# Performance work log

Hardware: AMD Instinct MI355X
Metric: run time of the kernel (lower is better)

Reference implementation:

```python
import jax, jax.numpy as jnp
import numpy as np

B, C, H, W = 4, 256, 64, 64
CI = 3
TEMPERATURE = 0.0001 * 5
EPS = 2.220446049250313e-16  # sys.float_info.epsilon


def _nearest_up4(x):
    # nn.Upsample(scale_factor=4, mode='nearest'): [B,C,H,W] -> [B,C,4H,4W]
    return jnp.repeat(jnp.repeat(x, 4, axis=2), 4, axis=3)


def _avg_pool2(x):
    # AvgPool2d(kernel=2, stride=2, pad=0)
    b, c, h, w = x.shape
    return x.reshape(b, c, h // 2, 2, w // 2, 2).mean(axis=(3, 5))


def _center_norm(feats):
    # subtract per-channel spatial mean, then L2-normalize over channels per position
    b, c, h, w = feats.shape
    t = feats.reshape(b, c, h * w)
    t = t - t.mean(axis=-1, keepdims=True)
    n = jnp.linalg.norm(t, axis=1, keepdims=True) + EPS
    return t / n  # [B,C,HW]


def setup_inputs() -> dict:
    key = jax.random.key(0)
    k1, k2, k3 = jax.random.split(key, 3)
    return {
        "x_feats": jax.random.normal(k1, (B, C, H, W), jnp.float32),
        "y_feats": jax.random.normal(k2, (B, C, H, W), jnp.float32),
        "y_img": jax.random.uniform(k3, (B, CI, 4 * H, 4 * W), jnp.float32),
    }


def reference(x_feats, y_feats, y_img):
    b, c, h, w = x_feats.shape
    hw = h * w
    theta = _center_norm(x_feats)  # [B,C,HW]
    phi = _center_norm(y_feats)    # [B,C,HW]
    f = jnp.einsum('bcm,bcn->bmn', theta, phi)  # dense correlation [B,HW,HW]
    loss_feat_pair = jnp.mean(jnp.abs(theta - phi))  # F.l1_loss(theta, phi)
    # WTA_scale_weight == 1 -> WTA branch bypassed, just temperature scaling
    f_wta = f / TEMPERATURE
    f_div_c = jax.nn.softmax(f_wta, axis=-1)  # [B,HW,HW]
    # warped features: f_div_C @ y_feats^T
    b_lab = y_feats.reshape(b, c, hw)
    y = jnp.einsum('bmn,bcn->bcm', f_div_c, b_lab).reshape(b, c, h, w)
    # soft-argmax coordinates
    xc = (jnp.arange(hw) % w).astype(x_feats.dtype)   # [HW]
    yc = (jnp.arange(hw) // w).astype(x_feats.dtype)  # [HW]
    coords_x = f_div_c @ xc  # [B,HW]
    coords_y = f_div_c @ yc  # [B,HW]
    coords1 = jnp.stack([coords_x, coords_y], axis=1).reshape(b, 2, h, w)
    coords0 = jnp.stack([xc, yc], axis=0).reshape(1, 2, h, w)
    flow = _nearest_up4(coords1 - coords0)  # [B,2,4H,4W]
    # image warping branch (y_img is not None)
    yi = _avg_pool2(_avg_pool2(y_img))  # [B,CI,H,W]
    ci = yi.shape[1]
    yi_flat = yi.reshape(b, ci, hw)
    y_img_attn = jnp.einsum('bmn,bcn->bmc', f_div_c, yi_flat)  # [B,HW,CI]
    f_div_c_v = jax.nn.softmax(jnp.swapaxes(f_wta, 1, 2), axis=-1)
    y_img_cyc = jnp.einsum('bmn,bnc->bcm', f_div_c_v, y_img_attn).reshape(b, ci, h, w)
    y_img_out = jnp.swapaxes(y_img_attn, 1, 2).reshape(b, ci, h, w)
    return (y, flow, _nearest_up4(y_img_out), _nearest_up4(y_img_cyc), loss_feat_pair)
```

## Files before the change

kernel.cpp:

```cpp
#include <hip/hip_runtime.h>
#include <math.h>

#define HW   4096
#define NCH  256
#define NB   4

constexpr float TEMP  = (float)(0.0001 * 5.0);
constexpr float INV_T = 1.0f / TEMP;
constexpr float EPSN  = 2.220446049250313e-16f;

typedef __attribute__((ext_vector_type(8))) _Float16 f16x8;
typedef __attribute__((ext_vector_type(4))) float    f32x4;

constexpr size_t OFF_YT    = 0;
constexpr size_t OFF_YI    = OFF_YT    + (size_t)NB*HW*NCH;
constexpr size_t OFF_MEAN  = OFF_YI    + (size_t)NB*3*HW;
constexpr size_t OFF_RNORM = OFF_MEAN  + (size_t)2*NB*NCH;
constexpr size_t OFF_NSQP  = OFF_RNORM + (size_t)2*NB*HW;
constexpr size_t OFF_F     = OFF_NSQP  + (size_t)2*NB*8*HW;
constexpr size_t OFF_YP    = OFF_F     + (size_t)HW*HW;
constexpr size_t OFF_ROWP  = OFF_YP;
constexpr size_t OFF_COLP  = OFF_YP + (size_t)32*7*HW;
constexpr size_t OFF_RMAX  = OFF_YP    + (size_t)8*NCH*HW;
constexpr size_t OFF_RSUM  = OFF_RMAX  + HW;
constexpr size_t OFF_CMAX  = OFF_RSUM  + HW;
constexpr size_t OFF_CSUM  = OFF_CMAX  + HW;
constexpr size_t OFF_COORD = OFF_CSUM  + HW;
constexpr size_t OFF_ATTN  = OFF_COORD + (size_t)NB*2*HW;
constexpr size_t OFF_CYC   = OFF_ATTN  + (size_t)NB*HW*3;
constexpr size_t OFF_CYCP  = OFF_CYC   + (size_t)NB*3*HW;
constexpr size_t OFF_LOSSP = OFF_CYCP  + (size_t)32*3*HW;
constexpr size_t OFF_F16   = OFF_LOSSP + 1024;

constexpr size_t OUT_Y    = 0;
constexpr size_t OUT_FLOW = (size_t)NB*NCH*HW;
constexpr size_t OUT_IMG  = OUT_FLOW + (size_t)NB*2*256*256;
constexpr size_t OUT_CYCO = OUT_IMG  + (size_t)NB*3*256*256;
constexpr size_t OUT_LOSS = OUT_CYCO + (size_t)NB*3*256*256;

__device__ __forceinline__ void gload16(const void* g, void* l) {
    __builtin_amdgcn_global_load_lds(
        (const __attribute__((address_space(1))) unsigned int*)g,
        (__attribute__((address_space(3))) unsigned int*)l, 16, 0, 0);
}

__global__ void mean_kernel(const float* __restrict__ xf, const float* __restrict__ yf,
                            float* __restrict__ means) {
    const float* src = (blockIdx.y == 0 ? xf : yf) + (size_t)blockIdx.x * HW;
    float s = 0.f;
    for (int i = threadIdx.x; i < HW; i += 256) s += src[i];
    __shared__ float red[256];
    red[threadIdx.x] = s; __syncthreads();
    for (int st = 128; st > 0; st >>= 1) {
        if (threadIdx.x < st) red[threadIdx.x] += red[threadIdx.x + st];
        __syncthreads();
    }
    if (threadIdx.x == 0) means[blockIdx.y * (NB*NCH) + blockIdx.x] = red[0] * (1.0f / HW);
}

__global__ void nsq_partial_kernel(const float* __restrict__ xf, const float* __restrict__ yf,
                                   const float* __restrict__ means, float* __restrict__ part) {
    int t = blockIdx.z >> 2, b = blockIdx.z & 3;
    int m = blockIdx.x * 256 + threadIdx.x;
    int c0 = blockIdx.y * 32;
    const float* src = (t == 0 ? xf : yf) + (size_t)b * NCH * HW;
    const float* mn = means + t * (NB*NCH) + b * NCH;
    float acc = 0.f;
    for (int c = c0; c < c0 + 32; ++c) {
        float v = src[(size_t)c * HW + m] - mn[c];
        acc += v * v;
    }
    part[(((size_t)t*NB + b) * 8 + blockIdx.y) * HW + m] = acc;
}

__global__ void nsq_combine_kernel(const float* __restrict__ part, float* __restrict__ rnorms) {
    int t = blockIdx.y >> 2, b = blockIdx.y & 3;
    int m = blockIdx.x * 256 + threadIdx.x;
    const float* p = part + ((size_t)t*NB + b) * 8 * HW + m;
    float s = 0.f;
    for (int k = 0; k < 8; ++k) s += p[(size_t)k * HW];
    rnorms[((size_t)t*NB + b) * HW + m] = 1.0f / (sqrtf(s) + EPSN);
}

__global__ void ycast_kernel(const float* __restrict__ yf, _Float16* __restrict__ yf16) {
    size_t i = ((size_t)blockIdx.x * 256 + threadIdx.x) * 8;
    const float4* s = (const float4*)(yf + i);
    float4 v0 = s[0], v1 = s[1];
    f16x8 o;
    o[0]=(_Float16)v0.x; o[1]=(_Float16)v0.y; o[2]=(_Float16)v0.z; o[3]=(_Float16)v0.w;
    o[4]=(_Float16)v1.x; o[5]=(_Float16)v1.y; o[6]=(_Float16)v1.z; o[7]=(_Float16)v1.w;
    *(f16x8*)(yf16 + i) = o;
}

__global__ void prep_kernel(const float* __restrict__ xf, const float* __restrict__ yf,
                            const float* __restrict__ means,
                            _Float16* __restrict__ th, _Float16* __restrict__ tl,
                            _Float16* __restrict__ ph, _Float16* __restrict__ pl, int b) {
    __shared__ float tile[32][33];
    int t = blockIdx.z;
    int c0 = blockIdx.x * 32, m0 = blockIdx.y * 32;
    const float* src = (t == 0 ? xf : yf) + (size_t)b * NCH * HW;
    const float* mn  = means + t * (NB*NCH) + b * NCH;
    int tx = threadIdx.x & 31, ty = threadIdx.x >> 5;
    for (int i = ty; i < 32; i += 8)
        tile[i][tx] = src[(size_t)(c0 + i) * HW + m0 + tx] - mn[c0 + i];
    __syncthreads();
    _Float16* H = (t == 0 ? th : ph);
    _Float16* L = (t == 0 ? tl : pl);
    for (int i = ty; i < 32; i += 8) {
        float v = tile[tx][i];
        _Float16 h = (_Float16)v;
        _Float16 l = (_Float16)(v - (float)h);
        H[(size_t)(m0 + i)*NCH + c0 + tx] = h;
        L[(size_t)(m0 + i)*NCH + c0 + tx] = l;
    }
}

__global__ void avgpool_kernel(const float* __restrict__ yimg, float* __restrict__ yi) {
    size_t idx = (size_t)blockIdx.x * 256 + threadIdx.x;
    int m  = (int)(idx & (HW - 1));
    int bc = (int)(idx >> 12);
    int h = m >> 6, w = m & 63;
    const float* p = yimg + (size_t)bc * 65536 + (size_t)(h*4) * 256 + w*4;
    float s = 0.f;
    #pragma unroll
    for (int dy = 0; dy < 4; ++dy) {
        #pragma unroll
        for (int dx = 0; dx < 4; ++dx) s += p[dy*256 + dx];
    }
    yi[idx] = s * (1.0f/16.0f);
}

__global__ __launch_bounds__(256) void gemm_f_kernel(
        const _Float16* __restrict__ th, const _Float16* __restrict__ tl,
        const _Float16* __restrict__ ph, const _Float16* __restrict__ pl,
        const float* __restrict__ rnorms, const float* __restrict__ yi,
        float* __restrict__ f, float* __restrict__ rowp, float* __restrict__ colp,
        int b) {
    __shared__ char lds[4][8192];
    int tid  = threadIdx.x;
    int lane = tid & 63;
    int w = tid >> 6, wm = w >> 1, wn = w & 1;
    int m0 = blockIdx.y * 128, n0 = blockIdx.x * 128;

    int o0 = tid * 16, o1 = o0 + 4096;
    int r0 = o0 >> 6, s0 = (o0 >> 4) & 3, g0 = s0 ^ ((r0 >> 1) & 3);
    int r1 = o1 >> 6, s1 = (o1 >> 4) & 3, g1 = s1 ^ ((r1 >> 1) & 3);
    size_t ga0 = (size_t)(n0 + r0)*NCH + g0*8;
    size_t ga1 = (size_t)(n0 + r1)*NCH + g1*8;
    size_t gb0 = (size_t)(m0 + r0)*NCH + g0*8;
    size_t gb1 = (size_t)(m0 + r1)*NCH + g1*8;

    int fra = wm*64 + (lane & 15);
    int frb = wn*64 + (lane & 15);
    int ks  = lane >> 4;

    f32x4 acc[4][4];
    #pragma unroll
    for (int i = 0; i < 4; ++i)
        #pragma unroll
        for (int j = 0; j < 4; ++j) acc[i][j] = (f32x4){0.f, 0.f, 0.f, 0.f};

    for (int kt = 0; kt < 8; ++kt) {
        int k0 = kt * 32;
        gload16(ph + ga0 + k0, &lds[0][o0]);
        gload16(ph + ga1 + k0, &lds[0][o1]);
        gload16(pl + ga0 + k0, &lds[1][o0]);
        gload16(pl + ga1 + k0, &lds[1][o1]);
        gload16(th + gb0 + k0, &lds[2][o0]);
        gload16(th + gb1 + k0, &lds[2][o1]);
        gload16(tl + gb0 + k0, &lds[3][o0]);
        gload16(tl + gb1 + k0, &lds[3][o1]);
        __syncthreads();

        f16x8 ah[4], al[4], bh[4], bl[4];
        #pragma unroll
        for (int i = 0; i < 4; ++i) {
            int rowa = fra + i*16;
            int offa = rowa*64 + ((ks ^ ((rowa >> 1) & 3)) << 4);
            ah[i] = *(const f16x8*)&lds[0][offa];
            al[i] = *(const f16x8*)&lds[1][offa];
            int rowb = frb + i*16;
            int offb = rowb*64 + ((ks ^ ((rowb >> 1) & 3)) << 4);
            bh[i] = *(const f16x8*)&lds[2][offb];
            bl[i] = *(const f16x8*)&lds[3][offb];
        }
        #pragma unroll
        for (int i = 0; i < 4; ++i)
            #pragma unroll
            for (int j = 0; j < 4; ++j) {
                acc[i][j] = __builtin_amdgcn_mfma_f32_16x16x32_f16(ah[i], bh[j], acc[i][j], 0, 0, 0);
                acc[i][j] = __builtin_amdgcn_mfma_f32_16x16x32_f16(ah[i], bl[j], acc[i][j], 0, 0, 0);
                acc[i][j] = __builtin_amdgcn_mfma_f32_16x16x32_f16(al[i], bh[j], acc[i][j], 0, 0, 0);
            }
        __syncthreads();
    }

    const float* rnx = rnorms + (size_t)b * HW;
    const float* rny = rnorms + (size_t)(NB + b) * HW;
    int mg[4];  float rxv[4];
    #pragma unroll
    for (int j = 0; j < 4; ++j) {
        mg[j] = m0 + wn*64 + j*16 + (lane & 15);
        rxv[j] = rnx[mg[j]];
    }
    int nl0 = wm*64 + (lane >> 4)*4;
    #pragma unroll
    for (int i = 0; i < 4; ++i)
        #pragma unroll
        for (int r = 0; r < 4; ++r) {
            float ry = rny[n0 + nl0 + i*16 + r];
            #pragma unroll
            for (int j = 0; j < 4; ++j) acc[i][j][r] *= rxv[j] * ry;
        }

    #pragma unroll
    for (int j = 0; j < 4; ++j)
        #pragma unroll
        for (int i = 0; i < 4; ++i)
            *(f32x4*)&f[(size_t)mg[j]*HW + n0 + nl0 + i*16] = acc[i][j];

    float* S     = (float*)&lds[0][0];
    float* rowm  = S;
    float* sums6 = S + 256;
    float* colm  = S + 1792;
    float* colsm = S + 2048;

    #pragma unroll
    for (int j = 0; j < 4; ++j) {
        float v = acc[0][j][0];
        #pragma unroll
        for (int i = 0; i < 4; ++i)
            #pragma unroll
            for (int r = 0; r < 4; ++r) v = fmaxf(v, acc[i][j][r]);
        v = fmaxf(v, __shfl_xor(v, 16));
        v = fmaxf(v, __shfl_xor(v, 32));
        if ((lane >> 4) == 0) rowm[wm*128 + wn*64 + j*16 + lane] = v;
    }
    #pragma unroll
    for (int i = 0; i < 4; ++i)
        #pragma unroll
        for (int r = 0; r < 4; ++r) {
            float v = fmaxf(fmaxf(acc[i][0][r], acc[i][1][r]),
                            fmaxf(acc[i][2][r], acc[i][3][r]));
            #pragma unroll
            for (int d = 1; d < 16; d <<= 1) v = fmaxf(v, __shfl_xor(v, d));
            if ((lane & 15) == 0) colm[wn*128 + wm*64 + i*16 + (lane >> 4)*4 + r] = v;
        }
    __syncthreads();

    float bm[4];
    #pragma unroll
    for (int j = 0; j < 4; ++j) {
        int ml = wn*64 + j*16 + (lane & 15);
        bm[j] = fmaxf(rowm[ml], rowm[128 + ml]);
    }
    float a6[4][6];
    #pragma unroll
    for (int j = 0; j < 4; ++j)
        #pragma unroll
        for (int q = 0; q < 6; ++q) a6[j][q] = 0.f;
    const float* yib = yi + (size_t)b * 3 * HW;
    #pragma unroll
    for (int i = 0; i < 4; ++i)
        #pragma unroll
        for (int r = 0; r < 4; ++r) {
            int ng = n0 + nl0 + i*16 + r;
            float xc = (float)(ng & 63), yc = (float)(ng >> 6);
            float y0 = yib[ng], y1 = yib[HW + ng], y2 = yib[2*HW + ng];
            #pragma unroll
            for (int j = 0; j < 4; ++j) {
                float e = __expf((acc[i][j][r] - bm[j]) * INV_T);
                a6[j][0] += e;      a6[j][1] += e*xc; a6[j][2] += e*yc;
                a6[j][3] += e*y0;   a6[j][4] += e*y1; a6[j][5] += e*y2;
            }
        }
    #pragma unroll
    for (int j = 0; j < 4; ++j)
        #pragma unroll
        for (int q = 0; q < 6; ++q) {
            float v = a6[j][q];
            v += __shfl_xor(v, 16);
            v += __shfl_xor(v, 32);
            if ((lane >> 4) == 0) sums6[(wm*128 + wn*64 + j*16 + lane)*6 + q] = v;
        }
    #pragma unroll
    for (int i = 0; i < 4; ++i)
        #pragma unroll
        for (int r = 0; r < 4; ++r) {
            int nl = wm*64 + i*16 + (lane >> 4)*4 + r;
            float cm = fmaxf(colm[nl], colm[128 + nl]);
            float cs = 0.f;
            #pragma unroll
            for (int j = 0; j < 4; ++j) cs += __expf((acc[i][j][r] - cm) * INV_T);
            #pragma unroll
            for (int d = 1; d < 16; d <<= 1) cs += __shfl_xor(cs, d);
            if ((lane & 15) == 0) colsm[wn*128 + nl] = cs;
        }
    __syncthreads();

    if (tid < 128) {
        int ml = tid;
        float m2 = fmaxf(rowm[ml], rowm[128 + ml]);
        rowp[((size_t)blockIdx.x*7 + 0)*HW + m0 + ml] = m2;
        #pragma unroll
        for (int q = 0; q < 6; ++q)
            rowp[((size_t)blockIdx.x*7 + 1 + q)*HW + m0 + ml] =
                sums6[ml*6 + q] + sums6[(128 + ml)*6 + q];
    } else {
        int nl = tid - 128;
        float c2 = fmaxf(colm[nl], colm[128 + nl]);
        colp[((size_t)blockIdx.y*2 + 0)*HW + n0 + nl] = c2;
        colp[((size_t)blockIdx.y*2 + 1)*HW + n0 + nl] = colsm[nl] + colsm[128 + nl];
    }
}

__global__ void row_combine_kernel(const float* __restrict__ rowp,
        float* __restrict__ rmax, float* __restrict__ rsuminv,
        float* __restrict__ coords, float* __restrict__ attn, int b) {
    int m = blockIdx.x * 256 + threadIdx.x;
    float gm = -3.0e38f;
    for (int t = 0; t < 32; ++t) gm = fmaxf(gm, rowp[((size_t)t*7)*HW + m]);
    float S=0, CX=0, CY=0, A0=0, A1=0, A2=0;
    for (int t = 0; t < 32; ++t) {
        const float* p = rowp + (size_t)t*7*HW + m;
        float wgt = __expf((p[0] - gm) * INV_T);
        S  += p[1*HW] * wgt; CX += p[2*HW] * wgt; CY += p[3*HW] * wgt;
        A0 += p[4*HW] * wgt; A1 += p[5*HW] * wgt; A2 += p[6*HW] * wgt;
    }
    float inv = 1.0f / S;
    rmax[m] = gm; rsuminv[m] = inv;
    coords[((size_t)b*2 + 0)*HW + m] = CX * inv;
    coords[((size_t)b*2 + 1)*HW + m] = CY * inv;
    attn[((size_t)b*HW + m)*3 + 0] = A0 * inv;
    attn[((size_t)b*HW + m)*3 + 1] = A1 * inv;
    attn[((size_t)b*HW + m)*3 + 2] = A2 * inv;
}

__global__ void col_combine_kernel(const float* __restrict__ colp,
        float* __restrict__ cmax, float* __restrict__ csuminv) {
    int n = blockIdx.x * 256 + threadIdx.x;
    float gm = -3.0e38f;
    for (int t = 0; t < 32; ++t) gm = fmaxf(gm, colp[((size_t)t*2)*HW + n]);
    float S = 0.f;
    for (int t = 0; t < 32; ++t) {
        const float* p = colp + (size_t)t*2*HW + n;
        S += p[1*HW] * __expf((p[0] - gm) * INV_T);
    }
    cmax[n] = gm;
    csuminv[n] = 1.0f / S;
}

__global__ __launch_bounds__(512) void gemm_y_kernel(const float* __restrict__ f,
        const float* __restrict__ rmax, const _Float16* __restrict__ yf16,
        float* __restrict__ yp, int b) {
    __shared__ __align__(16) char ldsA[8192];
    __shared__ __align__(16) char ldsB[16384];
    int tid  = threadIdx.x;
    int lane = tid & 63;
    int w = tid >> 6, wm = w >> 2, wn = w & 3;
    int m0 = blockIdx.x * 128;
    int ks = blockIdx.y;
    const _Float16* Yb = yf16 + (size_t)b * NCH * HW;

    int ar = tid >> 2, akc = tid & 3;
    int aoff = ar*64 + ((akc ^ ((ar >> 1) & 3)) << 4);
    float arm = rmax[m0 + ar];
    const float* frow = f + (size_t)(m0 + ar)*HW + akc*8;

    int o0 = tid*16, o1 = o0 + 8192;
    int br0 = o0 >> 6, bs0 = (o0 >> 4) & 3, bg0 = bs0 ^ ((br0 >> 1) & 3);
    int br1 = o1 >> 6, bs1 = (o1 >> 4) & 3, bg1 = bs1 ^ ((br1 >> 1) & 3);
    size_t gb0 = (size_t)br0*HW + bg0*8;
    size_t gb1 = (size_t)br1*HW + bg1*8;

    int fra = wm*64 + (lane & 15);
    int frb = wn*64 + (lane & 15);
    int kslot = lane >> 4;

    f32x4 acc[4][4];
    #pragma unroll
    for (int i = 0; i < 4; ++i)
        #pragma unroll
        for (int j = 0; j < 4; ++j) acc[i][j] = (f32x4){0.f, 0.f, 0.f, 0.f};

    for (int k0 = ks*512; k0 < ks*512 + 512; k0 += 32) {
        gload16(Yb + gb0 + k0, &ldsB[o0]);
        gload16(Yb + gb1 + k0, &ldsB[o1]);
        const float4* fp = (const float4*)(frow + k0);
        float4 v0 = fp[0], v1 = fp[1];
        f16x8 pk;
        pk[0] = (_Float16)__expf((v0.x - arm) * INV_T);
        pk[1] = (_Float16)__expf((v0.y - arm) * INV_T);
        pk[2] = (_Float16)__expf((v0.z - arm) * INV_T);
        pk[3] = (_Float16)__expf((v0.w - arm) * INV_T);
        pk[4] = (_Float16)__expf((v1.x - arm) * INV_T);
        pk[5] = (_Float16)__expf((v1.y - arm) * INV_T);
        pk[6] = (_Float16)__expf((v1.z - arm) * INV_T);
        pk[7] = (_Float16)__expf((v1.w - arm) * INV_T);
        *(f16x8*)&ldsA[aoff] = pk;
        __syncthreads();

        f16x8 af[4], bf[4];
        #pragma unroll
        for (int i = 0; i < 4; ++i) {
            int rowa = fra + i*16;
            af[i] = *(const f16x8*)&ldsA[rowa*64 + ((kslot ^ ((rowa >> 1) & 3)) << 4)];
            int rowb = frb + i*16;
            bf[i] = *(const f16x8*)&ldsB[rowb*64 + ((kslot ^ ((rowb >> 1) & 3)) << 4)];
        }
        #pragma unroll
        for (int i = 0; i < 4; ++i)
            #pragma unroll
            for (int j = 0; j < 4; ++j)
                acc[i][j] = __builtin_amdgcn_mfma_f32_16x16x32_f16(af[i], bf[j], acc[i][j], 0, 0, 0);
        __syncthreads();
    }

    #pragma unroll
    for (int i = 0; i < 4; ++i) {
        int m = m0 + wm*64 + i*16 + (lane >> 4) * 4;
        #pragma unroll
        for (int j = 0; j < 4; ++j) {
            int c = wn*64 + j*16 + (lane & 15);
            *(f32x4*)(yp + ((size_t)ks*NCH + c)*HW + m) = acc[i][j];
        }
    }
}

__global__ void ycombine_kernel(const float* __restrict__ yp, const float* __restrict__ rsuminv,
                                float* __restrict__ out, int b) {
    size_t idx = (size_t)blockIdx.x * 256 + threadIdx.x;
    int m = (int)(idx & (HW - 1));
    float s = 0.f;
    #pragma unroll
    for (int k = 0; k < 8; ++k) s += yp[(size_t)k*NCH*HW + idx];
    out[OUT_Y + (size_t)b*NCH*HW + idx] = s * rsuminv[m];
}

__global__ __launch_bounds__(256) void cyc_partial_kernel(const float* __restrict__ f,
        const float* __restrict__ cmax, const float* __restrict__ attn,
        float* __restrict__ part, int b) {
    __shared__ float at[128*3];
    int i  = blockIdx.x * 256 + threadIdx.x;
    int j0 = blockIdx.y * 128;
    for (int k = threadIdx.x; k < 384; k += 256)
        at[k] = attn[((size_t)b*HW + j0)*3 + k];
    __syncthreads();
    float cm = cmax[i];
    float a0=0, a1=0, a2=0;
    for (int jj = 0; jj < 128; ++jj) {
        float e = __expf((f[(size_t)(j0+jj)*HW + i] - cm) * INV_T);
        a0 = fmaf(e, at[jj*3+0], a0);
        a1 = fmaf(e, at[jj*3+1], a1);
        a2 = fmaf(e, at[jj*3+2], a2);
    }
    part[((size_t)blockIdx.y*3 + 0)*HW + i] = a0;
    part[((size_t)blockIdx.y*3 + 1)*HW + i] = a1;
    part[((size_t)blockIdx.y*3 + 2)*HW + i] = a2;
}

__global__ void cyc_combine_kernel(const float* __restrict__ part, const float* __restrict__ csuminv,
                                   float* __restrict__ cyc, int b) {
    int i = blockIdx.x * 256 + threadIdx.x;
    int c = blockIdx.y;
    float s = 0.f;
    for (int k = 0; k < 32; ++k) s += part[((size_t)k*3 + c)*HW + i];
    cyc[((size_t)b*3 + c)*HW + i] = s * csuminv[i];
}

__global__ void flow_kernel(const float* __restrict__ coords, float* __restrict__ out) {
    size_t idx = (size_t)blockIdx.x * 256 + threadIdx.x;
    int x4 = (int)(idx & 255);
    int y4 = (int)((idx >> 8) & 255);
    int ch = (int)((idx >> 16) & 1);
    int b  = (int)(idx >> 17);
    int w = x4 >> 2, h = y4 >> 2;
    int m = h*64 + w;
    float c1 = coords[((size_t)b*2 + ch)*HW + m];
    float c0 = (ch == 0) ? (float)w : (float)h;
    out[OUT_FLOW + idx] = c1 - c0;
}

__global__ void imgout_kernel(const float* __restrict__ attn, const float* __restrict__ cyc,
                              float* __restrict__ out) {
    size_t idx = (size_t)blockIdx.x * 256 + threadIdx.x;
    int x4 = (int)(idx & 255);
    int y4 = (int)((idx >> 8) & 255);
    int rest = (int)(idx >> 16);
    int ch = rest % 3, b = rest / 3;
    int m = (y4 >> 2)*64 + (x4 >> 2);
    out[OUT_IMG  + idx] = attn[((size_t)b*HW + m)*3 + ch];
    out[OUT_CYCO + idx] = cyc[((size_t)b*3 + ch)*HW + m];
}

__global__ void loss_partial_kernel(const float* __restrict__ xf, const float* __restrict__ yf,
                                    const float* __restrict__ means, const float* __restrict__ rnorms,
                                    float* __restrict__ part) {
    __shared__ float red[256];
    size_t base = (size_t)blockIdx.x * 4096;
    float s = 0.f;
    for (int k = 0; k < 16; ++k) {
        size_t id = base + (size_t)k*256 + threadIdx.x;
        int m  = (int)(id & (HW - 1));
        int bc = (int)(id >> 12);
        int b  = bc >> 8;
        float th = (xf[id] - means[bc])          * rnorms[(size_t)b*HW + m];
        float ph = (yf[id] - means[NB*NCH + bc]) * rnorms[(size_t)(NB + b)*HW + m];
        s += fabsf(th - ph);
    }
    red[threadIdx.x] = s; __syncthreads();
    for (int st = 128; st > 0; st >>= 1) {
        if (threadIdx.x < st) red[threadIdx.x] += red[threadIdx.x + st];
        __syncthreads();
    }
    if (threadIdx.x == 0) part[blockIdx.x] = red[0];
}

__global__ void loss_final_kernel(const float* __restrict__ part, float* __restrict__ out) {
    __shared__ float red[256];
    float s = 0.f;
    for (int k = threadIdx.x; k < 1024; k += 256) s += part[k];
    red[threadIdx.x] = s; __syncthreads();
    for (int st = 128; st > 0; st >>= 1) {
        if (threadIdx.x < st) red[threadIdx.x] += red[threadIdx.x + st];
        __syncthreads();
    }
    if (threadIdx.x == 0) out[OUT_LOSS] = red[0] * (1.0f / 4194304.0f);
}

extern "C" void kernel_launch(void* const* d_in, const int* in_sizes, int n_in,
                              void* d_out, int out_size, void* d_ws, size_t ws_size,
                              hipStream_t stream) {
    (void)in_sizes; (void)n_in; (void)out_size; (void)ws_size;
    const float* xf   = (const float*)d_in[0];
    const float* yf   = (const float*)d_in[1];
    const float* yimg = (const float*)d_in[2];
    float* out = (float*)d_out;
    float* ws  = (float*)d_ws;

    _Float16* yf16 = (_Float16*)(ws + OFF_YT);
    float* yi      = ws + OFF_YI;
    float* means   = ws + OFF_MEAN;
    float* rnorms  = ws + OFF_RNORM;
    float* nsqp    = ws + OFF_NSQP;
    float* fbuf    = ws + OFF_F;
    float* yp      = ws + OFF_YP;
    float* rowp    = ws + OFF_ROWP;
    float* colp    = ws + OFF_COLP;
    float* rmax    = ws + OFF_RMAX;
    float* rsuminv = ws + OFF_RSUM;
    float* cmax    = ws + OFF_CMAX;
    float* csuminv = ws + OFF_CSUM;
    float* coords  = ws + OFF_COORD;
    float* attn    = ws + OFF_ATTN;
    float* cyc     = ws + OFF_CYC;
    float* cycp    = ws + OFF_CYCP;
    float* lossp   = ws + OFF_LOSSP;
    _Float16* th = (_Float16*)(ws + OFF_F16);
    _Float16* tl = th + (size_t)HW*NCH;
    _Float16* ph = tl + (size_t)HW*NCH;
    _Float16* pl = ph + (size_t)HW*NCH;

    mean_kernel        <<<dim3(NB*NCH, 2),   256, 0, stream>>>(xf, yf, means);
    nsq_partial_kernel <<<dim3(16, 8, 8),    256, 0, stream>>>(xf, yf, means, nsqp);
    nsq_combine_kernel <<<dim3(16, 8),       256, 0, stream>>>(nsqp, rnorms);
    ycast_kernel       <<<2048,              256, 0, stream>>>(yf, yf16);
    avgpool_kernel     <<<NB*3*HW/256,       256, 0, stream>>>(yimg, yi);

    for (int b = 0; b < NB; ++b) {
        prep_kernel        <<<dim3(8, 128, 2), 256, 0, stream>>>(xf, yf, means, th, tl, ph, pl, b);
        gemm_f_kernel      <<<dim3(32, 32),    256, 0, stream>>>(th, tl, ph, pl, rnorms, yi,
                                                                 fbuf, rowp, colp, b);
        row_combine_kernel <<<16,              256, 0, stream>>>(rowp, rmax, rsuminv, coords, attn, b);
        col_combine_kernel <<<16,              256, 0, stream>>>(colp, cmax, csuminv);
        gemm_y_kernel      <<<dim3(32, 8),     512, 0, stream>>>(fbuf, rmax, yf16, yp, b);
        ycombine_kernel    <<<NCH*HW/256,      256, 0, stream>>>(yp, rsuminv, out, b);
        cyc_partial_kernel <<<dim3(16, 32),    256, 0, stream>>>(fbuf, cmax, attn, cycp, b);
        cyc_combine_kernel <<<dim3(16, 3),     256, 0, stream>>>(cycp, csuminv, cyc, b);
    }

    flow_kernel        <<<NB*2*65536/256, 256, 0, stream>>>(coords, out);
    imgout_kernel      <<<NB*3*65536/256, 256, 0, stream>>>(attn, cyc, out);
    loss_partial_kernel<<<1024,           256, 0, stream>>>(xf, yf, means, rnorms, lossp);
    loss_final_kernel  <<<1,              256, 0, stream>>>(lossp, out);
}
```

Measured before the change: 540.0 us.

## Enlarge correlation GEMM tile to 256x256 with 8 waves and staged epilogue

The split-fp16 correlation GEMM now uses 256x256 output tiles with 512 threads (each wave computing 128x64), which halves the number of partial row/column softmax statistics and the combine-kernel loop counts. The epilogue stages the y_img slice into shared memory and merges the column-exp pass into the row-exp loop, so acc is swept one fewer time. The cost is heavier register pressure (32 accumulators per lane) and only 256 blocks per batch, which may leave some of the GPU's compute units underused.

```diff
diff --git a/kernel.cpp b/kernel.cpp
--- a/kernel.cpp
+++ b/kernel.cpp
@@ -131,19 +131,22 @@
     yi[idx] = s * (1.0f/16.0f);
 }
 
-__global__ __launch_bounds__(256) void gemm_f_kernel(
+__global__ __launch_bounds__(512) void gemm_f_kernel(
         const _Float16* __restrict__ th, const _Float16* __restrict__ tl,
         const _Float16* __restrict__ ph, const _Float16* __restrict__ pl,
         const float* __restrict__ rnorms, const float* __restrict__ yi,
         float* __restrict__ f, float* __restrict__ rowp, float* __restrict__ colp,
         int b) {
-    __shared__ char lds[4][8192];
+    __shared__ __align__(16) char lds[4][16384];
     int tid  = threadIdx.x;
     int lane = tid & 63;
-    int w = tid >> 6, wm = w >> 1, wn = w & 1;
-    int m0 = blockIdx.y * 128, n0 = blockIdx.x * 128;
-
-    int o0 = tid * 16, o1 = o0 + 4096;
+    int g    = lane >> 4;
+    int w    = tid >> 6;
+    int wN   = w >> 2;
+    int wM   = w & 3;
+    int n0 = blockIdx.x * 256, m0 = blockIdx.y * 256;
+
+    int o0 = tid * 16, o1 = o0 + 8192;
     int r0 = o0 >> 6, s0 = (o0 >> 4) & 3, g0 = s0 ^ ((r0 >> 1) & 3);
     int r1 = o1 >> 6, s1 = (o1 >> 4) & 3, g1 = s1 ^ ((r1 >> 1) & 3);
     size_t ga0 = (size_t)(n0 + r0)*NCH + g0*8;
@@ -151,13 +154,12 @@
     size_t gb0 = (size_t)(m0 + r0)*NCH + g0*8;
     size_t gb1 = (size_t)(m0 + r1)*NCH + g1*8;
 
-    int fra = wm*64 + (lane & 15);
-    int frb = wn*64 + (lane & 15);
-    int ks  = lane >> 4;
-
-    f32x4 acc[4][4];
-    #pragma unroll
-    for (int i = 0; i < 4; ++i)
+    int fra = wN*128 + (lane & 15);
+    int frb = wM*64  + (lane & 15);
+
+    f32x4 acc[8][4];
+    #pragma unroll
+    for (int i = 0; i < 8; ++i)
         #pragma unroll
         for (int j = 0; j < 4; ++j) acc[i][j] = (f32x4){0.f, 0.f, 0.f, 0.f};
 
@@ -173,43 +175,44 @@
         gload16(tl + gb1 + k0, &lds[3][o1]);
         __syncthreads();
 
-        f16x8 ah[4], al[4], bh[4], bl[4];
-        #pragma unroll
-        for (int i = 0; i < 4; ++i) {
+        f16x8 bh[4], bl[4];
+        #pragma unroll
+        for (int j = 0; j < 4; ++j) {
+            int rowb = frb + j*16;
+            int offb = rowb*64 + ((g ^ ((rowb >> 1) & 3)) << 4);
+            bh[j] = *(const f16x8*)&lds[2][offb];
+            bl[j] = *(const f16x8*)&lds[3][offb];
+        }
+        #pragma unroll
+        for (int i = 0; i < 8; ++i) {
             int rowa = fra + i*16;
-            int offa = rowa*64 + ((ks ^ ((rowa >> 1) & 3)) << 4);
-            ah[i] = *(const f16x8*)&lds[0][offa];
-            al[i] = *(const f16x8*)&lds[1][offa];
-            int rowb = frb + i*16;
-            int offb = rowb*64 + ((ks ^ ((rowb >> 1) & 3)) << 4);
-            bh[i] = *(const f16x8*)&lds[2][offb];
-            bl[i] = *(const f16x8*)&lds[3][offb];
-        }
-        #pragma unroll
-        for (int i = 0; i < 4; ++i)
+            int offa = rowa*64 + ((g ^ ((rowa >> 1) & 3)) << 4);
+            f16x8 ah = *(const f16x8*)&lds[0][offa];
+            f16x8 al = *(const f16x8*)&lds[1][offa];
             #pragma unroll
             for (int j = 0; j < 4; ++j) {
-                acc[i][j] = __builtin_amdgcn_mfma_f32_16x16x32_f16(ah[i], bh[j], acc[i][j], 0, 0, 0);
-                acc[i][j] = __builtin_amdgcn_mfma_f32_16x16x32_f16(ah[i], bl[j], acc[i][j], 0, 0, 0);
-                acc[i][j] = __builtin_amdgcn_mfma_f32_16x16x32_f16(al[i], bh[j], acc[i][j], 0, 0, 0);
+                acc[i][j] = __builtin_amdgcn_mfma_f32_16x16x32_f16(ah, bh[j], acc[i][j], 0, 0, 0);
+                acc[i][j] = __builtin_amdgcn_mfma_f32_16x16x32_f16(ah, bl[j], acc[i][j], 0, 0, 0);
+                acc[i][j] = __builtin_amdgcn_mfma_f32_16x16x32_f16(al, bh[j], acc[i][j], 0, 0, 0);
             }
+        }
         __syncthreads();
     }
 
     const float* rnx = rnorms + (size_t)b * HW;
     const float* rny = rnorms + (size_t)(NB + b) * HW;
-    int mg[4];  float rxv[4];
+    int mg[4]; float rxv[4];
     #pragma unroll
     for (int j = 0; j < 4; ++j) {
-        mg[j] = m0 + wn*64 + j*16 + (lane & 15);
+        mg[j] = m0 + wM*64 + j*16 + (lane & 15);
         rxv[j] = rnx[mg[j]];
     }
-    int nl0 = wm*64 + (lane >> 4)*4;
-    #pragma unroll
-    for (int i = 0; i < 4; ++i)
+    int nlb = wN*128 + g*4;
+    #pragma unroll
+    for (int i = 0; i < 8; ++i)
         #pragma unroll
         for (int r = 0; r < 4; ++r) {
-            float ry = rny[n0 + nl0 + i*16 + r];
+            float ry = rny[n0 + nlb + i*16 + r];
             #pragma unroll
             for (int j = 0; j < 4; ++j) acc[i][j][r] *= rxv[j] * ry;
         }
@@ -217,63 +220,82 @@
     #pragma unroll
     for (int j = 0; j < 4; ++j)
         #pragma unroll
-        for (int i = 0; i < 4; ++i)
-            *(f32x4*)&f[(size_t)mg[j]*HW + n0 + nl0 + i*16] = acc[i][j];
-
-    float* S     = (float*)&lds[0][0];
-    float* rowm  = S;
-    float* sums6 = S + 256;
-    float* colm  = S + 1792;
-    float* colsm = S + 2048;
-
+        for (int i = 0; i < 8; ++i)
+            *(f32x4*)&f[(size_t)mg[j]*HW + n0 + nlb + i*16] = acc[i][j];
+
+    float* yiL = (float*)&lds[0][0];
+    float* rmL = yiL + 768;
+    float* cmL = rmL + 512;
+    float* rsL = cmL + 1024;
+    float* csL = rsL + 3072;
+
+    {
+        const float* yib = yi + (size_t)b * 3 * HW;
+        for (int k = tid; k < 768; k += 512) {
+            int ch = k >> 8, nn = k & 255;
+            yiL[k] = yib[(size_t)ch*HW + n0 + nn];
+        }
+    }
     #pragma unroll
     for (int j = 0; j < 4; ++j) {
         float v = acc[0][j][0];
         #pragma unroll
-        for (int i = 0; i < 4; ++i)
+        for (int i = 0; i < 8; ++i)
             #pragma unroll
             for (int r = 0; r < 4; ++r) v = fmaxf(v, acc[i][j][r]);
         v = fmaxf(v, __shfl_xor(v, 16));
         v = fmaxf(v, __shfl_xor(v, 32));
-        if ((lane >> 4) == 0) rowm[wm*128 + wn*64 + j*16 + lane] = v;
-    }
-    #pragma unroll
-    for (int i = 0; i < 4; ++i)
+        if (lane < 16) rmL[wN*256 + wM*64 + j*16 + lane] = v;
+    }
+    #pragma unroll
+    for (int i = 0; i < 8; ++i)
         #pragma unroll
         for (int r = 0; r < 4; ++r) {
             float v = fmaxf(fmaxf(acc[i][0][r], acc[i][1][r]),
                             fmaxf(acc[i][2][r], acc[i][3][r]));
             #pragma unroll
             for (int d = 1; d < 16; d <<= 1) v = fmaxf(v, __shfl_xor(v, d));
-            if ((lane & 15) == 0) colm[wn*128 + wm*64 + i*16 + (lane >> 4)*4 + r] = v;
+            if ((lane & 15) == 0) cmL[wM*256 + nlb + i*16 + r] = v;
         }
     __syncthreads();
 
+    if (tid < 256) {
+        rmL[tid] = fmaxf(rmL[tid], rmL[256 + tid]);
+    } else {
+        int n = tid - 256;
+        cmL[n] = fmaxf(fmaxf(cmL[n], cmL[256 + n]), fmaxf(cmL[512 + n], cmL[768 + n]));
+    }
+    __syncthreads();
+
     float bm[4];
     #pragma unroll
-    for (int j = 0; j < 4; ++j) {
-        int ml = wn*64 + j*16 + (lane & 15);
-        bm[j] = fmaxf(rowm[ml], rowm[128 + ml]);
-    }
+    for (int j = 0; j < 4; ++j) bm[j] = rmL[wM*64 + j*16 + (lane & 15)];
     float a6[4][6];
     #pragma unroll
     for (int j = 0; j < 4; ++j)
         #pragma unroll
         for (int q = 0; q < 6; ++q) a6[j][q] = 0.f;
-    const float* yib = yi + (size_t)b * 3 * HW;
-    #pragma unroll
-    for (int i = 0; i < 4; ++i)
+    #pragma unroll
+    for (int i = 0; i < 8; ++i)
         #pragma unroll
         for (int r = 0; r < 4; ++r) {
-            int ng = n0 + nl0 + i*16 + r;
+            int nl = nlb + i*16 + r;
+            int ng = n0 + nl;
             float xc = (float)(ng & 63), yc = (float)(ng >> 6);
-            float y0 = yib[ng], y1 = yib[HW + ng], y2 = yib[2*HW + ng];
+            float y0 = yiL[nl], y1 = yiL[256 + nl], y2 = yiL[512 + nl];
+            float cm = cmL[nl];
+            float cs = 0.f;
             #pragma unroll
             for (int j = 0; j < 4; ++j) {
-                float e = __expf((acc[i][j][r] - bm[j]) * INV_T);
+                float av = acc[i][j][r];
+                float e = __expf((av - bm[j]) * INV_T);
                 a6[j][0] += e;      a6[j][1] += e*xc; a6[j][2] += e*yc;
                 a6[j][3] += e*y0;   a6[j][4] += e*y1; a6[j][5] += e*y2;
+                cs += __expf((av - cm) * INV_T);
             }
+            #pragma unroll
+            for (int d = 1; d < 16; d <<= 1) cs += __shfl_xor(cs, d);
+            if ((lane & 15) == 0) csL[wM*256 + nl] = cs;
         }
     #pragma unroll
     for (int j = 0; j < 4; ++j)
@@ -282,36 +304,22 @@
             float v = a6[j][q];
             v += __shfl_xor(v, 16);
             v += __shfl_xor(v, 32);
-            if ((lane >> 4) == 0) sums6[(wm*128 + wn*64 + j*16 + lane)*6 + q] = v;
-        }
-    #pragma unroll
-    for (int i = 0; i < 4; ++i)
-        #pragma unroll
-        for (int r = 0; r < 4; ++r) {
-            int nl = wm*64 + i*16 + (lane >> 4)*4 + r;
-            float cm = fmaxf(colm[nl], colm[128 + nl]);
-            float cs = 0.f;
-            #pragma unroll
-            for (int j = 0; j < 4; ++j) cs += __expf((acc[i][j][r] - cm) * INV_T);
-            #pragma unroll
-            for (int d = 1; d < 16; d <<= 1) cs += __shfl_xor(cs, d);
-            if ((lane & 15) == 0) colsm[wn*128 + nl] = cs;
+            if (lane < 16) rsL[(wN*256 + wM*64 + j*16 + lane)*6 + q] = v;
         }
     __syncthreads();
 
-    if (tid < 128) {
+    if (tid < 256) {
         int ml = tid;
-        float m2 = fmaxf(rowm[ml], rowm[128 + ml]);
-        rowp[((size_t)blockIdx.x*7 + 0)*HW + m0 + ml] = m2;
+        rowp[((size_t)blockIdx.x*7 + 0)*HW + m0 + ml] = rmL[ml];
         #pragma unroll
         for (int q = 0; q < 6; ++q)
             rowp[((size_t)blockIdx.x*7 + 1 + q)*HW + m0 + ml] =
-                sums6[ml*6 + q] + sums6[(128 + ml)*6 + q];
+                rsL[ml*6 + q] + rsL[(256 + ml)*6 + q];
     } else {
-        int nl = tid - 128;
-        float c2 = fmaxf(colm[nl], colm[128 + nl]);
-        colp[((size_t)blockIdx.y*2 + 0)*HW + n0 + nl] = c2;
-        colp[((size_t)blockIdx.y*2 + 1)*HW + n0 + nl] = colsm[nl] + colsm[128 + nl];
+        int nl = tid - 256;
+        colp[((size_t)blockIdx.y*2 + 0)*HW + n0 + nl] = cmL[nl];
+        colp[((size_t)blockIdx.y*2 + 1)*HW + n0 + nl] =
+            csL[nl] + csL[256 + nl] + csL[512 + nl] + csL[768 + nl];
     }
 }
 
@@ -320,9 +328,9 @@
         float* __restrict__ coords, float* __restrict__ attn, int b) {
     int m = blockIdx.x * 256 + threadIdx.x;
     float gm = -3.0e38f;
-    for (int t = 0; t < 32; ++t) gm = fmaxf(gm, rowp[((size_t)t*7)*HW + m]);
+    for (int t = 0; t < 16; ++t) gm = fmaxf(gm, rowp[((size_t)t*7)*HW + m]);
     float S=0, CX=0, CY=0, A0=0, A1=0, A2=0;
-    for (int t = 0; t < 32; ++t) {
+    for (int t = 0; t < 16; ++t) {
         const float* p = rowp + (size_t)t*7*HW + m;
         float wgt = __expf((p[0] - gm) * INV_T);
         S  += p[1*HW] * wgt; CX += p[2*HW] * wgt; CY += p[3*HW] * wgt;
@@ -341,9 +349,9 @@
         float* __restrict__ cmax, float* __restrict__ csuminv) {
     int n = blockIdx.x * 256 + threadIdx.x;
     float gm = -3.0e38f;
-    for (int t = 0; t < 32; ++t) gm = fmaxf(gm, colp[((size_t)t*2)*HW + n]);
+    for (int t = 0; t < 16; ++t) gm = fmaxf(gm, colp[((size_t)t*2)*HW + n]);
     float S = 0.f;
-    for (int t = 0; t < 32; ++t) {
+    for (int t = 0; t < 16; ++t) {
         const float* p = colp + (size_t)t*2*HW + n;
         S += p[1*HW] * __expf((p[0] - gm) * INV_T);
     }
@@ -570,7 +578,7 @@
 
     for (int b = 0; b < NB; ++b) {
         prep_kernel        <<<dim3(8, 128, 2), 256, 0, stream>>>(xf, yf, means, th, tl, ph, pl, b);
-        gemm_f_kernel      <<<dim3(32, 32),    256, 0, stream>>>(th, tl, ph, pl, rnorms, yi,
+        gemm_f_kernel      <<<dim3(16, 16),    512, 0, stream>>>(th, tl, ph, pl, rnorms, yi,
                                                                  fbuf, rowp, colp, b);
         row_combine_kernel <<<16,              256, 0, stream>>>(rowp, rmax, rsuminv, coords, attn, b);
         col_combine_kernel <<<16,              256, 0, stream>>>(colp, cmax, csuminv);
```

New measurement: 561.4 us. +4.0%, slower.
